# Optimization experiments

Measured on AMD Instinct MI355X. Metric: run time of the kernel, lower is better.

Reference implementation:

```python
import jax, jax.numpy as jnp
import numpy as np

EPS = 1e-5  # clamp epsilon; also used to fill the background slab (as in the torch code)


def setup_inputs() -> dict:
    key = jax.random.key(0)
    # smoothed voxel occupancies in [0, 1): [B, D, H, W]
    voxels = jax.random.uniform(key, (16, 128, 128, 128), dtype=jnp.float32)
    return {"voxels": voxels}


def reference(voxels) -> jnp.ndarray:
    # voxels: [B, D, H, W] occupancy grid; D is the ray/depth axis.
    B, D, H, W = voxels.shape
    o = jnp.clip(voxels, EPS, 1.0 - EPS)
    log_free = jnp.log(1.0 - o)          # log prob ray passes each cell
    log_occ = jnp.log(o)                 # log prob ray terminates at each cell
    # cumulative transmittance in log space along depth
    cum_free = jnp.cumsum(log_free, axis=1)            # [B, D, H, W]
    eps_slab = jnp.full((B, 1, H, W), EPS, dtype=voxels.dtype)
    r1 = jnp.concatenate([eps_slab, cum_free], axis=1)  # [B, D+1, H, W]
    r2 = jnp.concatenate([log_occ, eps_slab], axis=1)   # [B, D+1, H, W]
    probs = jnp.exp(r1 + r2)                             # ray termination probs
    # drop background cell, project along depth, flip vertically
    return jnp.flip(probs[:, :-1].sum(axis=1), axis=1)   # [B, H, W]
```

## Files before the change

kernel.cpp:

```cpp
#include <hip/hip_runtime.h>


#define EPS 1e-5f
#define EXP_EPS 1.0000100000500002f

#define B_ 16
#define D_ 128
#define H_ 128
#define W_ 128

__device__ __forceinline__ float clampo(float v) {
    return fminf(fmaxf(v, EPS), 1.0f - EPS);
}

__global__ __launch_bounds__(128) void ray_term_kernel(const float* __restrict__ vox,
                                                       float* __restrict__ out) {
    const int w4 = threadIdx.x;
    const int h  = blockIdx.x * blockDim.y + threadIdx.y;
    const int b  = blockIdx.y;

    const float4* __restrict__ src =
        (const float4*)(vox + ((size_t)b * D_ * H_ + (size_t)h) * W_) + w4;
    const int dstride = H_ * W_ / 4;

    float4 v0 = src[0];
    float o0 = clampo(v0.x), o1 = clampo(v0.y), o2 = clampo(v0.z), o3 = clampo(v0.w);
    float a0 = o0 * EXP_EPS, a1 = o1 * EXP_EPS, a2 = o2 * EXP_EPS, a3 = o3 * EXP_EPS;
    float T0 = 1.0f - o0, T1 = 1.0f - o1, T2 = 1.0f - o2, T3 = 1.0f - o3;

    #pragma unroll 8
    for (int d = 1; d < D_; ++d) {
        float4 v = src[(size_t)d * dstride];
        o0 = clampo(v.x); o1 = clampo(v.y); o2 = clampo(v.z); o3 = clampo(v.w);
        a0 = fmaf(o0, T0, a0); T0 *= (1.0f - o0);
        a1 = fmaf(o1, T1, a1); T1 *= (1.0f - o1);
        a2 = fmaf(o2, T2, a2); T2 *= (1.0f - o2);
        a3 = fmaf(o3, T3, a3); T3 *= (1.0f - o3);
    }

    float* __restrict__ dst =
        out + ((size_t)b * H_ + (size_t)(H_ - 1 - h)) * W_ + 4 * w4;
    *(float4*)dst = make_float4(a0, a1, a2, a3);
}

extern "C" void kernel_launch(void* const* d_in, const int* in_sizes, int n_in,
                              void* d_out, int out_size, void* d_ws, size_t ws_size,
                              hipStream_t stream) {
    const float* vox = (const float*)d_in[0];
    float* out = (float*)d_out;
    dim3 block(32, 4, 1);
    dim3 grid(H_ / 4, B_, 1);
    ray_term_kernel<<<grid, block, 0, stream>>>(vox, out);
}
```

Baseline: 184.0 us.

## Split depth scan into chunks and combine partial transmittance in second kernel

Splits the depth axis into four chunks so each block scans only a quarter of the rays, writing partial accumulated probability and transmittance to workspace. A second kernel combines chunks associatively and writes the flipped output. This raises the number of blocks in flight to hide memory latency of the long serial per-thread loop, at the cost of extra workspace traffic and a second launch.

Measured after the change: 191.1 us. 3.9% more time.

```diff
diff --git a/kernel.cpp b/kernel.cpp
--- a/kernel.cpp
+++ b/kernel.cpp
@@ -8,47 +8,96 @@
 #define D_ 128
 #define H_ 128
 #define W_ 128
+#define C_ 4
+#define DC_ (D_ / C_)
+#define Q_ (B_ * H_ * W_ / 4)
 
 __device__ __forceinline__ float clampo(float v) {
     return fminf(fmaxf(v, EPS), 1.0f - EPS);
 }
 
-__global__ __launch_bounds__(128) void ray_term_kernel(const float* __restrict__ vox,
-                                                       float* __restrict__ out) {
+
+__global__ __launch_bounds__(128) void ray_chunk_kernel(const float* __restrict__ vox,
+                                                        float4* __restrict__ ws) {
     const int w4 = threadIdx.x;
     const int h  = blockIdx.x * blockDim.y + threadIdx.y;
     const int b  = blockIdx.y;
+    const int c  = blockIdx.z;
 
     const float4* __restrict__ src =
-        (const float4*)(vox + ((size_t)b * D_ * H_ + (size_t)h) * W_) + w4;
+        (const float4*)(vox + (((size_t)b * D_ + (size_t)c * DC_) * H_ + (size_t)h) * W_) + w4;
     const int dstride = H_ * W_ / 4;
 
-    float4 v0 = src[0];
-    float o0 = clampo(v0.x), o1 = clampo(v0.y), o2 = clampo(v0.z), o3 = clampo(v0.w);
-    float a0 = o0 * EXP_EPS, a1 = o1 * EXP_EPS, a2 = o2 * EXP_EPS, a3 = o3 * EXP_EPS;
-    float T0 = 1.0f - o0, T1 = 1.0f - o1, T2 = 1.0f - o2, T3 = 1.0f - o3;
+    float a0 = 0.f, a1 = 0.f, a2 = 0.f, a3 = 0.f;
+    float T0 = 1.f, T1 = 1.f, T2 = 1.f, T3 = 1.f;
 
-    #pragma unroll 8
-    for (int d = 1; d < D_; ++d) {
-        float4 v = src[(size_t)d * dstride];
-        o0 = clampo(v.x); o1 = clampo(v.y); o2 = clampo(v.z); o3 = clampo(v.w);
-        a0 = fmaf(o0, T0, a0); T0 *= (1.0f - o0);
-        a1 = fmaf(o1, T1, a1); T1 *= (1.0f - o1);
-        a2 = fmaf(o2, T2, a2); T2 *= (1.0f - o2);
-        a3 = fmaf(o3, T3, a3); T3 *= (1.0f - o3);
+    if (c == 0) {
+        float4 v = src[0];
+        float o0 = clampo(v.x), o1 = clampo(v.y), o2 = clampo(v.z), o3 = clampo(v.w);
+        a0 = o0 * EXP_EPS; a1 = o1 * EXP_EPS; a2 = o2 * EXP_EPS; a3 = o3 * EXP_EPS;
+        T0 = 1.f - o0; T1 = 1.f - o1; T2 = 1.f - o2; T3 = 1.f - o3;
+        #pragma unroll 8
+        for (int d = 1; d < DC_; ++d) {
+            float4 v2 = src[(size_t)d * dstride];
+            float p0 = clampo(v2.x), p1 = clampo(v2.y), p2 = clampo(v2.z), p3 = clampo(v2.w);
+            a0 = fmaf(p0, T0, a0); T0 *= (1.f - p0);
+            a1 = fmaf(p1, T1, a1); T1 *= (1.f - p1);
+            a2 = fmaf(p2, T2, a2); T2 *= (1.f - p2);
+            a3 = fmaf(p3, T3, a3); T3 *= (1.f - p3);
+        }
+    } else {
+        #pragma unroll 8
+        for (int d = 0; d < DC_; ++d) {
+            float4 v2 = src[(size_t)d * dstride];
+            float p0 = clampo(v2.x), p1 = clampo(v2.y), p2 = clampo(v2.z), p3 = clampo(v2.w);
+            a0 = fmaf(p0, T0, a0); T0 *= (1.f - p0);
+            a1 = fmaf(p1, T1, a1); T1 *= (1.f - p1);
+            a2 = fmaf(p2, T2, a2); T2 *= (1.f - p2);
+            a3 = fmaf(p3, T3, a3); T3 *= (1.f - p3);
+        }
     }
 
-    float* __restrict__ dst =
-        out + ((size_t)b * H_ + (size_t)(H_ - 1 - h)) * W_ + 4 * w4;
-    *(float4*)dst = make_float4(a0, a1, a2, a3);
+    const size_t idx = ((size_t)b * H_ + (size_t)h) * (W_ / 4) + w4;
+    ws[(size_t)(2 * c) * Q_ + idx]     = make_float4(a0, a1, a2, a3);
+    ws[(size_t)(2 * c + 1) * Q_ + idx] = make_float4(T0, T1, T2, T3);
+}
+
+__device__ __forceinline__ float4 f4_fma(float4 t, float4 r, float4 a) {
+    return make_float4(fmaf(t.x, r.x, a.x), fmaf(t.y, r.y, a.y),
+                       fmaf(t.z, r.z, a.z), fmaf(t.w, r.w, a.w));
+}
+
+__global__ __launch_bounds__(256) void ray_combine_kernel(const float4* __restrict__ ws,
+                                                          float4* __restrict__ out) {
+    const int idx = blockIdx.x * 256 + threadIdx.x;
+    const int w4s = W_ / 4;
+    const int w4 = idx & (w4s - 1);
+    const int hb = idx / w4s;
+    const int h = hb & (H_ - 1);
+    const int b = hb / H_;
+
+    float4 a0 = ws[0 * Q_ + idx], t0 = ws[1 * Q_ + idx];
+    float4 a1 = ws[2 * Q_ + idx], t1 = ws[3 * Q_ + idx];
+    float4 a2 = ws[4 * Q_ + idx], t2 = ws[5 * Q_ + idx];
+    float4 a3 = ws[6 * Q_ + idx];
+
+    float4 r = f4_fma(t2, a3, a2);
+    r = f4_fma(t1, r, a1);
+    r = f4_fma(t0, r, a0);
+
+    out[((size_t)b * H_ + (size_t)(H_ - 1 - h)) * w4s + w4] = r;
 }
 
 extern "C" void kernel_launch(void* const* d_in, const int* in_sizes, int n_in,
                               void* d_out, int out_size, void* d_ws, size_t ws_size,
                               hipStream_t stream) {
     const float* vox = (const float*)d_in[0];
-    float* out = (float*)d_out;
-    dim3 block(32, 4, 1);
-    dim3 grid(H_ / 4, B_, 1);
-    ray_term_kernel<<<grid, block, 0, stream>>>(vox, out);
+    float4* ws = (float4*)d_ws;
+    float4* out = (float4*)d_out;
+
+    dim3 block1(32, 4, 1);
+    dim3 grid1(H_ / 4, B_, C_);
+    ray_chunk_kernel<<<grid1, block1, 0, stream>>>(vox, ws);
+
+    ray_combine_kernel<<<Q_ / 256, 256, 0, stream>>>(ws, out);
 }
```

## Split depth recurrence across threads and combine partial transmittance via shared memory

Applied to the files above, without the earlier changes.

Each ray's depth loop is divided into four chunks handled by separate threads, each computing a partial accumulated probability and transmittance product. The partials are combined in shared memory with the associative compositing rule, and only the first chunk writes the output. This increases the number of waves and in-flight loads to hide memory latency of the serial depth loop, at the cost of a block barrier and some idle threads during the combine.

New measurement: 186.0 us. No clear change (+1.1%).

```diff
diff --git a/kernel.cpp b/kernel.cpp
--- a/kernel.cpp
+++ b/kernel.cpp
@@ -8,39 +8,77 @@
 #define D_ 128
 #define H_ 128
 #define W_ 128
+#define C_ 4
+#define DC_ (D_ / C_)
+#define BY_ 2
 
 __device__ __forceinline__ float clampo(float v) {
     return fminf(fmaxf(v, EPS), 1.0f - EPS);
 }
 
-__global__ __launch_bounds__(128) void ray_term_kernel(const float* __restrict__ vox,
+__device__ __forceinline__ float4 f4_fma(float4 t, float4 r, float4 a) {
+    return make_float4(fmaf(t.x, r.x, a.x), fmaf(t.y, r.y, a.y),
+                       fmaf(t.z, r.z, a.z), fmaf(t.w, r.w, a.w));
+}
+
+__global__ __launch_bounds__(256) void ray_term_kernel(const float* __restrict__ vox,
                                                        float* __restrict__ out) {
     const int w4 = threadIdx.x;
-    const int h  = blockIdx.x * blockDim.y + threadIdx.y;
+    const int hy = threadIdx.y;
+    const int c  = threadIdx.z;
+    const int h  = blockIdx.x * BY_ + hy;
     const int b  = blockIdx.y;
 
     const float4* __restrict__ src =
-        (const float4*)(vox + ((size_t)b * D_ * H_ + (size_t)h) * W_) + w4;
+        (const float4*)(vox + (((size_t)b * D_ + (size_t)c * DC_) * H_ + (size_t)h) * W_) + w4;
     const int dstride = H_ * W_ / 4;
 
-    float4 v0 = src[0];
-    float o0 = clampo(v0.x), o1 = clampo(v0.y), o2 = clampo(v0.z), o3 = clampo(v0.w);
-    float a0 = o0 * EXP_EPS, a1 = o1 * EXP_EPS, a2 = o2 * EXP_EPS, a3 = o3 * EXP_EPS;
-    float T0 = 1.0f - o0, T1 = 1.0f - o1, T2 = 1.0f - o2, T3 = 1.0f - o3;
+    float a0, a1, a2, a3, T0, T1, T2, T3;
+    int dstart;
+    if (c == 0) {
+        float4 v = src[0];
+        float o0 = clampo(v.x), o1 = clampo(v.y), o2 = clampo(v.z), o3 = clampo(v.w);
+        a0 = o0 * EXP_EPS; a1 = o1 * EXP_EPS; a2 = o2 * EXP_EPS; a3 = o3 * EXP_EPS;
+        T0 = 1.f - o0; T1 = 1.f - o1; T2 = 1.f - o2; T3 = 1.f - o3;
+        dstart = 1;
+    } else {
+        a0 = a1 = a2 = a3 = 0.f;
+        T0 = T1 = T2 = T3 = 1.f;
+        dstart = 0;
+    }
 
     #pragma unroll 8
-    for (int d = 1; d < D_; ++d) {
+    for (int d = dstart; d < DC_; ++d) {
         float4 v = src[(size_t)d * dstride];
-        o0 = clampo(v.x); o1 = clampo(v.y); o2 = clampo(v.z); o3 = clampo(v.w);
-        a0 = fmaf(o0, T0, a0); T0 *= (1.0f - o0);
-        a1 = fmaf(o1, T1, a1); T1 *= (1.0f - o1);
-        a2 = fmaf(o2, T2, a2); T2 *= (1.0f - o2);
-        a3 = fmaf(o3, T3, a3); T3 *= (1.0f - o3);
+        float p0 = clampo(v.x), p1 = clampo(v.y), p2 = clampo(v.z), p3 = clampo(v.w);
+        a0 = fmaf(p0, T0, a0); T0 *= (1.f - p0);
+        a1 = fmaf(p1, T1, a1); T1 *= (1.f - p1);
+        a2 = fmaf(p2, T2, a2); T2 *= (1.f - p2);
+        a3 = fmaf(p3, T3, a3); T3 *= (1.f - p3);
     }
 
-    float* __restrict__ dst =
-        out + ((size_t)b * H_ + (size_t)(H_ - 1 - h)) * W_ + 4 * w4;
-    *(float4*)dst = make_float4(a0, a1, a2, a3);
+    __shared__ float4 a_l[C_ - 1][BY_][32];
+    __shared__ float4 t_l[C_ - 2][BY_][32];
+    if (c >= 1) {
+        a_l[c - 1][hy][w4] = make_float4(a0, a1, a2, a3);
+        if (c <= 2) t_l[c - 1][hy][w4] = make_float4(T0, T1, T2, T3);
+    }
+    __syncthreads();
+
+    if (c == 0) {
+        float4 A1 = a_l[0][hy][w4], TT1 = t_l[0][hy][w4];
+        float4 A2 = a_l[1][hy][w4], TT2 = t_l[1][hy][w4];
+        float4 A3 = a_l[2][hy][w4];
+        float4 r = f4_fma(TT2, A3, A2);
+        r = f4_fma(TT1, r, A1);
+        float4 myA = make_float4(a0, a1, a2, a3);
+        float4 myT = make_float4(T0, T1, T2, T3);
+        r = f4_fma(myT, r, myA);
+
+        float* __restrict__ dst =
+            out + ((size_t)b * H_ + (size_t)(H_ - 1 - h)) * W_ + 4 * w4;
+        *(float4*)dst = r;
+    }
 }
 
 extern "C" void kernel_launch(void* const* d_in, const int* in_sizes, int n_in,
@@ -48,7 +86,7 @@
                               hipStream_t stream) {
     const float* vox = (const float*)d_in[0];
     float* out = (float*)d_out;
-    dim3 block(32, 4, 1);
-    dim3 grid(H_ / 4, B_, 1);
+    dim3 block(32, BY_, C_);
+    dim3 grid(H_ / BY_, B_, 1);
     ray_term_kernel<<<grid, block, 0, stream>>>(vox, out);
 }
```
